# Kernel optimization log

Measured on AMD Instinct MI355X. Metric: run time of the kernel, lower is better.

The kernel has to match this reference:

```python
import jax, jax.numpy as jnp
import numpy as np

# --- config constants (from init_kwargs) ---
ALPHA = 0.05; SIGMA = 0.2; THETA = 0.3; A = 0.02; B_PAR = 0.1; RHO = 0.5
MULT = 2.0          # config.x_range_final[1]
GAMMA = 0.5         # power-utility exponent: u(x,r)=r*x^g/g, ux=r*x^(g-1)
N_STEPS = 100; T_FINAL = 1.0; DT = T_FINAL / N_STEPS
HID = 64; BATCH = 16384
PEN_SCALE = 100.0; LOWER = 1e-6


def _mlp(W1, b1, W2, b2, W3, b3, s):
    # tiny FeedForwardSubNet: 3 -> HID -> HID -> 1, tanh activations
    h = jnp.tanh(s @ W1 + b1)
    h = jnp.tanh(h @ W2 + b2)
    return h @ W3 + b3


def _penalise(v):
    # penalise_range(v, lower): quadratic hinge below `lower`
    return PEN_SCALE * jnp.square(jnp.maximum(LOWER - v, 0.0))


def setup_inputs() -> dict:
    key = jax.random.key(0)
    ks = jax.random.split(key, 16)
    dw = jax.random.normal(ks[0], (BATCH, 1, N_STEPS), dtype=jnp.float32) * float(np.sqrt(DT))
    X0 = jnp.ones((1,), jnp.float32)
    R0 = jnp.ones((1,), jnp.float32)
    def w(k, shape, fan):
        return jax.random.normal(k, shape, jnp.float32) / np.float32(np.sqrt(fan))
    inp = {"dw": dw, "X0": X0, "R0": R0,
           "pW1": w(ks[1], (3, HID), 3), "pb1": jnp.zeros((HID,), jnp.float32),
           "pW2": w(ks[2], (HID, HID), HID), "pb2": jnp.zeros((HID,), jnp.float32),
           "pW3": w(ks[3], (HID, 1), HID), "pb3": jnp.zeros((1,), jnp.float32),
           "qW1": w(ks[4], (3, HID), 3), "qb1": jnp.zeros((HID,), jnp.float32),
           "qW2": w(ks[5], (HID, HID), HID), "qb2": jnp.zeros((HID,), jnp.float32),
           "qW3": w(ks[6], (HID, 1), HID), "qb3": jnp.zeros((1,), jnp.float32)}
    return inp


def reference(dw, X0, R0, pW1, pb1, pW2, pb2, pW3, pb3, qW1, qb1, qW2, qb2, qW3, qb3):
    Bn = dw.shape[0]
    ones = jnp.ones((Bn, 1), dw.dtype)
    times = jnp.arange(N_STEPS + 1, dtype=dw.dtype) * DT   # [N+1]
    x0 = ones * X0
    R0v = ones * R0
    b_eff = float(np.sign(RHO)) * B_PAR

    # p_0 and dp_0 = d p_0 / d x (per-sample, rowwise independent net)
    def p_of_x(xx):
        st = jnp.concatenate([MULT * times[0] * ones, xx, R0v], 1)
        return _mlp(pW1, pb1, pW2, pb2, pW3, pb3, st)
    p0, p_vjp = jax.vjp(p_of_x, x0)
    (dp0,) = p_vjp(jnp.ones_like(p0))
    pi0 = _mlp(qW1, qb1, qW2, qb2, qW3, qb3,
               jnp.concatenate([MULT * times[0] * ones, x0, R0v], 1))

    dw_t = jnp.transpose(dw, (2, 0, 1))          # [N, B, 1]
    upd = jnp.arange(N_STEPS) < (N_STEPS - 1)    # pi not updated at last step

    def step(carry, inp):
        x, min_x, W, pi = carry
        dwi, t_next, u = inp
        x = x + x * ALPHA * DT + pi * SIGMA * THETA * DT + pi * SIGMA * dwi
        min_x = jnp.minimum(x, min_x)
        W = W + dwi
        Rv = R0v * jnp.exp((A - 0.5 * b_eff ** 2) * t_next + b_eff * W)
        p = p0 * jnp.exp(-(ALPHA + 0.5 * THETA ** 2) * t_next - THETA * W)
        st = jnp.concatenate([MULT * t_next * jnp.ones_like(x), x, Rv], 1)
        pi_new = _mlp(qW1, qb1, qW2, qb2, qW3, qb3, st)
        pi = jnp.where(u, pi_new, pi)
        return (x, min_x, W, pi), (x, Rv, pi, -p)

    (xf, min_x, Wf, pif), (xs, Rs, pis, dMs) = jax.lax.scan(
        step, (x0, x0, jnp.zeros_like(x0), pi0), (dw_t, times[1:], upd))

    # stacked process data, matching tf.concat-over-axis-0 ordering: [(N+1)*B, 1]
    x_all  = jnp.concatenate([x0[None], xs], 0).reshape(-1, 1)
    r_all  = jnp.concatenate([R0v[None], Rs], 0).reshape(-1, 1)
    pi_all = jnp.concatenate([pi0[None], pis], 0).reshape(-1, 1)
    dM_all = jnp.concatenate([(-p0)[None], dMs], 0).reshape(-1, 1)
    dM2_all = jnp.tile(-dp0, (N_STEPS + 1, 1))
    proc = jnp.concatenate([x_all, r_all, pi_all, dM_all, dM2_all], 1)  # [(N+1)*B, 5]

    # losses (non_concave = False branch)
    p_fin = -dMs[-1]
    R_fin = Rs[-1]
    xc = jnp.maximum(xf, LOWER)
    ux = R_fin * xc ** (GAMMA - 1.0)
    u_val = R_fin * xc ** GAMMA / GAMMA
    pen = _penalise(min_x)
    loss_p = jnp.mean(jnp.square(p_fin + ux) + pen)
    loss_pi = loss_p + jnp.mean(-u_val + pen)

    return jnp.concatenate([proc.reshape(-1), jnp.stack([loss_p, loss_pi])])
```

## Files before the change

### kernel.cpp

```cpp
#include <hip/hip_runtime.h>
#include <hip/hip_bf16.h>
#include <math.h>

#define NSTEP 100
#define BATCH 16384
#define MB 16
#define NBLK (BATCH/MB)
#define NT 64

#define C_ALPHA 0.05f
#define C_SIGMA 0.2f
#define C_THETA 0.3f
#define C_DT    0.01f
#define C_LOWER 1e-6f
#define C_PEN   100.0f
#define LOG2E   1.4426950408889634f
#define TSCALE  (2.0f * LOG2E)
#define CRT ( 0.015f * C_DT * LOG2E)
#define CRW ( 0.1f * LOG2E)
#define CPT (-0.095f * C_DT * LOG2E)
#define CPW (-0.3f * LOG2E)

typedef __attribute__((ext_vector_type(8))) short bf16x8;
typedef __attribute__((ext_vector_type(4))) float f32x4;

__device__ __forceinline__ float tanh_pre(float zs) {
    float e = __builtin_amdgcn_exp2f(zs);
    return 1.0f - 2.0f * __builtin_amdgcn_rcpf(e + 1.0f);
}
__device__ __forceinline__ unsigned f2bf_u(float f) {
    unsigned u = __float_as_uint(f);
    return (u + 0x7FFFu + ((u >> 16) & 1u)) >> 16;
}
__device__ __forceinline__ unsigned pack_bf16(float a, float b) {
    union { __hip_bfloat162 h; unsigned u; } cv;
    cv.h = __float22bfloat162_rn(make_float2(a, b));
    return cv.u;
}
__device__ __forceinline__ float dpp_row_sum16(float v) {
    int t;
    t = __builtin_amdgcn_update_dpp(0, __float_as_int(v), 0x128, 0xF, 0xF, true);
    v += __int_as_float(t);
    t = __builtin_amdgcn_update_dpp(0, __float_as_int(v), 0x124, 0xF, 0xF, true);
    v += __int_as_float(t);
    t = __builtin_amdgcn_update_dpp(0, __float_as_int(v), 0x122, 0xF, 0xF, true);
    v += __int_as_float(t);
    t = __builtin_amdgcn_update_dpp(0, __float_as_int(v), 0x121, 0xF, 0xF, true);
    v += __int_as_float(t);
    return v;
}

__global__ __launch_bounds__(NT, 1) void fused_kernel(
        const float* __restrict__ dw, const float* __restrict__ X0,
        const float* __restrict__ R0,
        const float* __restrict__ pW1, const float* __restrict__ pb1,
        const float* __restrict__ pW2, const float* __restrict__ pb2,
        const float* __restrict__ pW3, const float* __restrict__ pb3,
        const float* __restrict__ qW1, const float* __restrict__ qb1,
        const float* __restrict__ qW2, const float* __restrict__ qb2,
        const float* __restrict__ qW3, const float* __restrict__ qb3,
        float* __restrict__ ws, float* __restrict__ out) {
    __shared__ __align__(16) unsigned short sW2T[64 * 72];
    __shared__ __align__(16) float sdw[MB * NSTEP];

    const int tid = threadIdx.x;
    const int lane = tid;
    const int b0 = blockIdx.x * MB;
    const int l15 = lane & 15, quad = lane >> 4;

    {
        const float4* g = (const float4*)(dw + (size_t)b0 * NSTEP);
        float4* s = (float4*)sdw;
        for (int u = tid; u < MB * NSTEP / 4; u += NT) s[u] = g[u];
    }
    for (int u4 = tid; u4 < 1024; u4 += NT) {
        float4 w = ((const float4*)qW2)[u4];
        int base = u4 * 4;
        int k = base >> 6, n = base & 63;
        sW2T[(n + 0) * 72 + k] = (unsigned short)f2bf_u(w.x * TSCALE);
        sW2T[(n + 1) * 72 + k] = (unsigned short)f2bf_u(w.y * TSCALE);
        sW2T[(n + 2) * 72 + k] = (unsigned short)f2bf_u(w.z * TSCALE);
        sW2T[(n + 3) * 72 + k] = (unsigned short)f2bf_u(w.w * TSCALE);
    }
    __syncthreads();

    bf16x8 Bf[4][2];
    #pragma unroll
    for (int nt = 0; nt < 4; nt++) {
        const unsigned short* rp = &sW2T[(nt * 16 + l15) * 72 + quad * 8];
        Bf[nt][0] = *(const bf16x8*)rp;
        Bf[nt][1] = *(const bf16x8*)(rp + 32);
    }
    float tco[16], w1xs[16], w1rs[16], b1s[16];
    {
        const int kq = quad * 8;
        #pragma unroll
        for (int j = 0; j < 8; j++) {
            tco[j]      = qW1[kq + j]        * (2.0f * C_DT * TSCALE);
            tco[8 + j]  = qW1[32 + kq + j]   * (2.0f * C_DT * TSCALE);
            w1xs[j]     = qW1[64 + kq + j]   * TSCALE;
            w1xs[8 + j] = qW1[96 + kq + j]   * TSCALE;
            w1rs[j]     = qW1[128 + kq + j]  * TSCALE;
            w1rs[8 + j] = qW1[160 + kq + j]  * TSCALE;
            b1s[j]      = qb1[kq + j]        * TSCALE;
            b1s[8 + j]  = qb1[32 + kq + j]   * TSCALE;
        }
    }
    f32x4 b2a[4];
    float w3c[4][4];
    #pragma unroll
    for (int nt = 0; nt < 4; nt++) {
        #pragma unroll
        for (int r = 0; r < 4; r++) {
            b2a[nt][r] = qb2[nt * 16 + quad * 4 + r] * TSCALE;
            w3c[nt][r] = qW3[nt * 16 + quad * 4 + r];
        }
    }
    const float b3 = qb3[0];
    const float X0v = X0[0], R0s = R0[0];

    float p0, dp0;
    {
        float pre = fmaf(pW1[64 + lane], X0v, fmaf(pW1[128 + lane], R0s, pb1[lane]));
        float h1 = tanh_pre(TSCALE * pre);
        float d1 = (1.0f - h1 * h1) * pW1[64 + lane];
        float a0 = pb2[lane], a1 = 0.f, a2 = 0.f, a3 = 0.f;
        float e0 = 0.f, e1 = 0.f, e2 = 0.f, e3 = 0.f;
        for (int i2 = 0; i2 < 64; i2 += 4) {
            float w0 = pW2[(i2 + 0) * 64 + lane];
            float w1 = pW2[(i2 + 1) * 64 + lane];
            float w2 = pW2[(i2 + 2) * 64 + lane];
            float w3 = pW2[(i2 + 3) * 64 + lane];
            a0 = fmaf(__shfl(h1, i2 + 0), w0, a0); e0 = fmaf(__shfl(d1, i2 + 0), w0, e0);
            a1 = fmaf(__shfl(h1, i2 + 1), w1, a1); e1 = fmaf(__shfl(d1, i2 + 1), w1, e1);
            a2 = fmaf(__shfl(h1, i2 + 2), w2, a2); e2 = fmaf(__shfl(d1, i2 + 2), w2, e2);
            a3 = fmaf(__shfl(h1, i2 + 3), w3, a3); e3 = fmaf(__shfl(d1, i2 + 3), w3, e3);
        }
        float pre2 = (a0 + a1) + (a2 + a3);
        float dpre2 = (e0 + e1) + (e2 + e3);
        float h2 = tanh_pre(TSCALE * pre2);
        float d2 = (1.0f - h2 * h2) * dpre2;
        float c1 = h2 * pW3[lane], c2 = d2 * pW3[lane];
        #pragma unroll
        for (int o = 1; o < 64; o <<= 1) {
            c1 += __shfl_xor(c1, o);
            c2 += __shfl_xor(c2, o);
        }
        p0 = c1 + pb3[0]; dp0 = c2;
    }

    auto qnet = [&](float fi, float xv, float rv) -> float {
        union { bf16x8 v; unsigned u[4]; } A0u, A1u;
        #pragma unroll
        for (int p = 0; p < 4; p++) {
            const int i0 = 2 * p, i1 = 2 * p + 1;
            float z0 = fmaf(w1rs[i0], rv, fmaf(w1xs[i0], xv, fmaf(tco[i0], fi, b1s[i0])));
            float z1 = fmaf(w1rs[i1], rv, fmaf(w1xs[i1], xv, fmaf(tco[i1], fi, b1s[i1])));
            A0u.u[p] = pack_bf16(tanh_pre(z0), tanh_pre(z1));
            float z2 = fmaf(w1rs[8 + i0], rv, fmaf(w1xs[8 + i0], xv, fmaf(tco[8 + i0], fi, b1s[8 + i0])));
            float z3 = fmaf(w1rs[8 + i1], rv, fmaf(w1xs[8 + i1], xv, fmaf(tco[8 + i1], fi, b1s[8 + i1])));
            A1u.u[p] = pack_bf16(tanh_pre(z2), tanh_pre(z3));
        }
        float ps0 = 0.f, ps1 = 0.f, ps2 = 0.f, ps3 = 0.f;
        #pragma unroll
        for (int nt = 0; nt < 4; nt++) {
            f32x4 a = b2a[nt];
            a = __builtin_amdgcn_mfma_f32_16x16x32_bf16(Bf[nt][0], A0u.v, a, 0, 0, 0);
            a = __builtin_amdgcn_mfma_f32_16x16x32_bf16(Bf[nt][1], A1u.v, a, 0, 0, 0);
            ps0 = fmaf(tanh_pre(a[0]), w3c[nt][0], ps0);
            ps1 = fmaf(tanh_pre(a[1]), w3c[nt][1], ps1);
            ps2 = fmaf(tanh_pre(a[2]), w3c[nt][2], ps2);
            ps3 = fmaf(tanh_pre(a[3]), w3c[nt][3], ps3);
        }
        float ps = (ps0 + ps1) + (ps2 + ps3);
        ps += __shfl_xor(ps, 16);
        ps += __shfl_xor(ps, 32);
        return ps + b3;
    };

    float x = X0v, Wsum = 0.0f, minx = X0v;
    float pi = qnet(0.0f, X0v, R0s);
    if (quad == 0) {
        size_t base = (size_t)(b0 + l15) * 5;
        out[base] = X0v; out[base + 1] = R0s; out[base + 2] = pi;
        out[base + 3] = -p0; out[base + 4] = -dp0;
    }

    float dw_next = sdw[l15 * NSTEP];
    #pragma unroll 1
    for (int i = 0; i < NSTEP - 1; i++) {
        const float fi = (float)(i + 1);
        float dwv = dw_next;
        dw_next = sdw[l15 * NSTEP + i + 1];
        float t = pi * C_SIGMA;
        x = fmaf(x, 1.0f + C_ALPHA * C_DT, fmaf(t, dwv, t * (C_THETA * C_DT)));
        minx = fminf(minx, x);
        Wsum += dwv;
        float R = R0s * __builtin_amdgcn_exp2f(fmaf(CRW, Wsum, CRT * fi));
        float pm = p0 * __builtin_amdgcn_exp2f(fmaf(CPW, Wsum, CPT * fi));
        float pin = qnet(fi, x, R);
        if (quad == 0) {
            size_t base = ((size_t)(i + 1) * BATCH + b0 + l15) * 5;
            out[base] = x; out[base + 1] = R; out[base + 2] = pin;
            out[base + 3] = -pm; out[base + 4] = -dp0;
        }
        pi = pin;
    }

    {
        float dwv = dw_next;
        float t = pi * C_SIGMA;
        x = fmaf(x, 1.0f + C_ALPHA * C_DT, fmaf(t, dwv, t * (C_THETA * C_DT)));
        minx = fminf(minx, x);
        Wsum += dwv;
        float Rf = R0s * __builtin_amdgcn_exp2f(fmaf(CRW, Wsum, CRT * (float)NSTEP));
        float pf = p0 * __builtin_amdgcn_exp2f(fmaf(CPW, Wsum, CPT * (float)NSTEP));
        if (quad == 0) {
            size_t base = ((size_t)NSTEP * BATCH + b0 + l15) * 5;
            out[base] = x; out[base + 1] = Rf; out[base + 2] = pi;
            out[base + 3] = -pf; out[base + 4] = -dp0;
        }
        float xc = fmaxf(x, C_LOWER);
        float ux = Rf * rsqrtf(xc);
        float uval = 2.0f * Rf * sqrtf(xc);
        float d = fmaxf(C_LOWER - minx, 0.0f);
        float pen = C_PEN * d * d;
        float t1 = pf + ux;
        float v1 = dpp_row_sum16(t1 * t1 + pen);
        float v2 = dpp_row_sum16(-uval + pen);
        if (lane == 0) {
            atomicAdd(&ws[3], v1);
            atomicAdd(&ws[4], v2);
            __threadfence();
            int old = atomicAdd((int*)(ws + 5), 1);
            if (old == NBLK - 1) {
                float lp = atomicAdd(&ws[3], 0.0f) * (1.0f / (float)BATCH);
                float lq = atomicAdd(&ws[4], 0.0f) * (1.0f / (float)BATCH);
                out[(size_t)(NSTEP + 1) * BATCH * 5] = lp;
                out[(size_t)(NSTEP + 1) * BATCH * 5 + 1] = lp + lq;
            }
        }
    }
}

extern "C" void kernel_launch(void* const* d_in, const int* in_sizes, int n_in,
                              void* d_out, int out_size, void* d_ws, size_t ws_size,
                              hipStream_t stream) {
    const float* dw  = (const float*)d_in[0];
    const float* X0  = (const float*)d_in[1];
    const float* R0  = (const float*)d_in[2];
    const float* pW1 = (const float*)d_in[3];
    const float* pb1 = (const float*)d_in[4];
    const float* pW2 = (const float*)d_in[5];
    const float* pb2 = (const float*)d_in[6];
    const float* pW3 = (const float*)d_in[7];
    const float* pb3 = (const float*)d_in[8];
    const float* qW1 = (const float*)d_in[9];
    const float* qb1 = (const float*)d_in[10];
    const float* qW2 = (const float*)d_in[11];
    const float* qb2 = (const float*)d_in[12];
    const float* qW3 = (const float*)d_in[13];
    const float* qb3 = (const float*)d_in[14];
    float* out = (float*)d_out;
    float* ws  = (float*)d_ws;

    hipMemsetAsync(d_ws, 0, 64, stream);
    fused_kernel<<<NBLK, NT, 0, stream>>>(dw, X0, R0, pW1, pb1, pW2, pb2, pW3, pb3,
                                          qW1, qb1, qW2, qb2, qW3, qb3, ws, out);
}
```

Baseline: 215.1 us.

## Split per-step Q-network across two wavefronts with LDS exchange

```diff
diff --git a/kernel.cpp b/kernel.cpp
--- a/kernel.cpp
+++ b/kernel.cpp
@@ -6,7 +6,7 @@
 #define BATCH 16384
 #define MB 16
 #define NBLK (BATCH/MB)
-#define NT 64
+#define NT 128
 
 #define C_ALPHA 0.05f
 #define C_SIGMA 0.2f
@@ -21,6 +21,8 @@
 #define CPT (-0.095f * C_DT * LOG2E)
 #define CPW (-0.3f * LOG2E)
 
+#define WG_BARRIER() asm volatile("s_waitcnt lgkmcnt(0)\n\ts_barrier" ::: "memory")
+
 typedef __attribute__((ext_vector_type(8))) short bf16x8;
 typedef __attribute__((ext_vector_type(4))) float f32x4;
 
@@ -50,7 +52,7 @@
     return v;
 }
 
-__global__ __launch_bounds__(NT, 1) void fused_kernel(
+__global__ __launch_bounds__(NT, 2) void fused_kernel(
         const float* __restrict__ dw, const float* __restrict__ X0,
         const float* __restrict__ R0,
         const float* __restrict__ pW1, const float* __restrict__ pb1,
@@ -62,59 +64,48 @@
         float* __restrict__ ws, float* __restrict__ out) {
     __shared__ __align__(16) unsigned short sW2T[64 * 72];
     __shared__ __align__(16) float sdw[MB * NSTEP];
+    __shared__ __align__(16) uint4 sA[2][2][64];
+    __shared__ __align__(16) float sP[2][2][16];
 
     const int tid = threadIdx.x;
-    const int lane = tid;
+    const int lane = tid & 63;
+    const int wv = tid >> 6;
     const int b0 = blockIdx.x * MB;
     const int l15 = lane & 15, quad = lane >> 4;
 
     {
         const float4* g = (const float4*)(dw + (size_t)b0 * NSTEP);
         float4* s = (float4*)sdw;
+        #pragma unroll
         for (int u = tid; u < MB * NSTEP / 4; u += NT) s[u] = g[u];
     }
-    for (int u4 = tid; u4 < 1024; u4 += NT) {
-        float4 w = ((const float4*)qW2)[u4];
-        int base = u4 * 4;
-        int k = base >> 6, n = base & 63;
-        sW2T[(n + 0) * 72 + k] = (unsigned short)f2bf_u(w.x * TSCALE);
-        sW2T[(n + 1) * 72 + k] = (unsigned short)f2bf_u(w.y * TSCALE);
-        sW2T[(n + 2) * 72 + k] = (unsigned short)f2bf_u(w.z * TSCALE);
-        sW2T[(n + 3) * 72 + k] = (unsigned short)f2bf_u(w.w * TSCALE);
+    for (int u = tid; u < 4096; u += NT) {
+        int k = u >> 6, n = u & 63;
+        sW2T[n * 72 + k] = (unsigned short)f2bf_u(qW2[u] * TSCALE);
     }
     __syncthreads();
 
-    bf16x8 Bf[4][2];
+    bf16x8 Bf[2][2];
     #pragma unroll
-    for (int nt = 0; nt < 4; nt++) {
-        const unsigned short* rp = &sW2T[(nt * 16 + l15) * 72 + quad * 8];
-        Bf[nt][0] = *(const bf16x8*)rp;
-        Bf[nt][1] = *(const bf16x8*)(rp + 32);
-    }
-    float tco[16], w1xs[16], w1rs[16], b1s[16];
-    {
-        const int kq = quad * 8;
-        #pragma unroll
-        for (int j = 0; j < 8; j++) {
-            tco[j]      = qW1[kq + j]        * (2.0f * C_DT * TSCALE);
-            tco[8 + j]  = qW1[32 + kq + j]   * (2.0f * C_DT * TSCALE);
-            w1xs[j]     = qW1[64 + kq + j]   * TSCALE;
-            w1xs[8 + j] = qW1[96 + kq + j]   * TSCALE;
-            w1rs[j]     = qW1[128 + kq + j]  * TSCALE;
-            w1rs[8 + j] = qW1[160 + kq + j]  * TSCALE;
-            b1s[j]      = qb1[kq + j]        * TSCALE;
-            b1s[8 + j]  = qb1[32 + kq + j]   * TSCALE;
-        }
-    }
-    f32x4 b2a[4];
-    float w3c[4][4];
+    for (int t = 0; t < 2; t++) {
+        const unsigned short* r = &sW2T[(wv * 32 + t * 16 + l15) * 72 + quad * 8];
+        Bf[t][0] = *(const bf16x8*)r;
+        Bf[t][1] = *(const bf16x8*)(r + 32);
+    }
+    float tco[8], w1xs[8], w1rs[8], b1s[8];
     #pragma unroll
-    for (int nt = 0; nt < 4; nt++) {
-        #pragma unroll
-        for (int r = 0; r < 4; r++) {
-            b2a[nt][r] = qb2[nt * 16 + quad * 4 + r] * TSCALE;
-            w3c[nt][r] = qW3[nt * 16 + quad * 4 + r];
-        }
+    for (int j = 0; j < 8; j++) {
+        int k = wv * 32 + quad * 8 + j;
+        tco[j]  = qW1[k] * (2.0f * C_DT * TSCALE);
+        w1xs[j] = qW1[64 + k] * TSCALE;
+        w1rs[j] = qW1[128 + k] * TSCALE;
+        b1s[j]  = qb1[k] * TSCALE;
+    }
+    float b2v[2], w3v[2];
+    #pragma unroll
+    for (int t = 0; t < 2; t++) {
+        b2v[t] = qb2[wv * 32 + t * 16 + l15] * TSCALE;
+        w3v[t] = qW3[wv * 32 + t * 16 + l15];
     }
     const float b3 = qb3[0];
     const float X0v = X0[0], R0s = R0[0];
@@ -149,38 +140,39 @@
         p0 = c1 + pb3[0]; dp0 = c2;
     }
 
-    auto qnet = [&](float fi, float xv, float rv) -> float {
-        union { bf16x8 v; unsigned u[4]; } A0u, A1u;
+    auto qnet = [&](int par, float fi, float xv, float rv) -> float {
+        union { uint4 u4; bf16x8 v; unsigned u[4]; } Aloc, Aoth;
         #pragma unroll
         for (int p = 0; p < 4; p++) {
             const int i0 = 2 * p, i1 = 2 * p + 1;
             float z0 = fmaf(w1rs[i0], rv, fmaf(w1xs[i0], xv, fmaf(tco[i0], fi, b1s[i0])));
             float z1 = fmaf(w1rs[i1], rv, fmaf(w1xs[i1], xv, fmaf(tco[i1], fi, b1s[i1])));
-            A0u.u[p] = pack_bf16(tanh_pre(z0), tanh_pre(z1));
-            float z2 = fmaf(w1rs[8 + i0], rv, fmaf(w1xs[8 + i0], xv, fmaf(tco[8 + i0], fi, b1s[8 + i0])));
-            float z3 = fmaf(w1rs[8 + i1], rv, fmaf(w1xs[8 + i1], xv, fmaf(tco[8 + i1], fi, b1s[8 + i1])));
-            A1u.u[p] = pack_bf16(tanh_pre(z2), tanh_pre(z3));
-        }
-        float ps0 = 0.f, ps1 = 0.f, ps2 = 0.f, ps3 = 0.f;
-        #pragma unroll
-        for (int nt = 0; nt < 4; nt++) {
-            f32x4 a = b2a[nt];
-            a = __builtin_amdgcn_mfma_f32_16x16x32_bf16(Bf[nt][0], A0u.v, a, 0, 0, 0);
-            a = __builtin_amdgcn_mfma_f32_16x16x32_bf16(Bf[nt][1], A1u.v, a, 0, 0, 0);
-            ps0 = fmaf(tanh_pre(a[0]), w3c[nt][0], ps0);
-            ps1 = fmaf(tanh_pre(a[1]), w3c[nt][1], ps1);
-            ps2 = fmaf(tanh_pre(a[2]), w3c[nt][2], ps2);
-            ps3 = fmaf(tanh_pre(a[3]), w3c[nt][3], ps3);
-        }
-        float ps = (ps0 + ps1) + (ps2 + ps3);
-        ps += __shfl_xor(ps, 16);
-        ps += __shfl_xor(ps, 32);
-        return ps + b3;
+            Aloc.u[p] = pack_bf16(tanh_pre(z0), tanh_pre(z1));
+        }
+        sA[par][wv][lane] = Aloc.u4;
+        WG_BARRIER();
+        Aoth.u4 = sA[par][1 - wv][lane];
+        bf16x8 A0 = (wv == 0) ? Aloc.v : Aoth.v;
+        bf16x8 A1 = (wv == 0) ? Aoth.v : Aloc.v;
+        f32x4 acc0 = {b2v[0], b2v[0], b2v[0], b2v[0]};
+        f32x4 acc1 = {b2v[1], b2v[1], b2v[1], b2v[1]};
+        acc0 = __builtin_amdgcn_mfma_f32_16x16x32_bf16(A0, Bf[0][0], acc0, 0, 0, 0);
+        acc1 = __builtin_amdgcn_mfma_f32_16x16x32_bf16(A0, Bf[1][0], acc1, 0, 0, 0);
+        acc0 = __builtin_amdgcn_mfma_f32_16x16x32_bf16(A1, Bf[0][1], acc0, 0, 0, 0);
+        acc1 = __builtin_amdgcn_mfma_f32_16x16x32_bf16(A1, Bf[1][1], acc1, 0, 0, 0);
+        f32x4 part;
+        #pragma unroll
+        for (int r = 0; r < 4; r++)
+            part[r] = dpp_row_sum16(
+                fmaf(tanh_pre(acc1[r]), w3v[1], tanh_pre(acc0[r]) * w3v[0]));
+        if (l15 == 0) *(f32x4*)&sP[par][wv][quad * 4] = part;
+        WG_BARRIER();
+        return sP[par][0][l15] + sP[par][1][l15] + b3;
     };
 
     float x = X0v, Wsum = 0.0f, minx = X0v;
-    float pi = qnet(0.0f, X0v, R0s);
-    if (quad == 0) {
+    float pi = qnet(0, 0.0f, X0v, R0s);
+    if (wv == 1 && quad == 0) {
         size_t base = (size_t)(b0 + l15) * 5;
         out[base] = X0v; out[base + 1] = R0s; out[base + 2] = pi;
         out[base + 3] = -p0; out[base + 4] = -dp0;
@@ -198,8 +190,8 @@
         Wsum += dwv;
         float R = R0s * __builtin_amdgcn_exp2f(fmaf(CRW, Wsum, CRT * fi));
         float pm = p0 * __builtin_amdgcn_exp2f(fmaf(CPW, Wsum, CPT * fi));
-        float pin = qnet(fi, x, R);
-        if (quad == 0) {
+        float pin = qnet((i + 1) & 1, fi, x, R);
+        if (wv == 1 && quad == 0) {
             size_t base = ((size_t)(i + 1) * BATCH + b0 + l15) * 5;
             out[base] = x; out[base + 1] = R; out[base + 2] = pin;
             out[base + 3] = -pm; out[base + 4] = -dp0;
@@ -215,29 +207,31 @@
         Wsum += dwv;
         float Rf = R0s * __builtin_amdgcn_exp2f(fmaf(CRW, Wsum, CRT * (float)NSTEP));
         float pf = p0 * __builtin_amdgcn_exp2f(fmaf(CPW, Wsum, CPT * (float)NSTEP));
-        if (quad == 0) {
+        if (wv == 1 && quad == 0) {
             size_t base = ((size_t)NSTEP * BATCH + b0 + l15) * 5;
             out[base] = x; out[base + 1] = Rf; out[base + 2] = pi;
             out[base + 3] = -pf; out[base + 4] = -dp0;
         }
-        float xc = fmaxf(x, C_LOWER);
-        float ux = Rf * rsqrtf(xc);
-        float uval = 2.0f * Rf * sqrtf(xc);
-        float d = fmaxf(C_LOWER - minx, 0.0f);
-        float pen = C_PEN * d * d;
-        float t1 = pf + ux;
-        float v1 = dpp_row_sum16(t1 * t1 + pen);
-        float v2 = dpp_row_sum16(-uval + pen);
-        if (lane == 0) {
-            atomicAdd(&ws[3], v1);
-            atomicAdd(&ws[4], v2);
-            __threadfence();
-            int old = atomicAdd((int*)(ws + 5), 1);
-            if (old == NBLK - 1) {
-                float lp = atomicAdd(&ws[3], 0.0f) * (1.0f / (float)BATCH);
-                float lq = atomicAdd(&ws[4], 0.0f) * (1.0f / (float)BATCH);
-                out[(size_t)(NSTEP + 1) * BATCH * 5] = lp;
-                out[(size_t)(NSTEP + 1) * BATCH * 5 + 1] = lp + lq;
+        if (wv == 0) {
+            float xc = fmaxf(x, C_LOWER);
+            float ux = Rf * rsqrtf(xc);
+            float uval = 2.0f * Rf * sqrtf(xc);
+            float d = fmaxf(C_LOWER - minx, 0.0f);
+            float pen = C_PEN * d * d;
+            float t1 = pf + ux;
+            float v1 = dpp_row_sum16(t1 * t1 + pen);
+            float v2 = dpp_row_sum16(-uval + pen);
+            if (lane == 0) {
+                atomicAdd(&ws[3], v1);
+                atomicAdd(&ws[4], v2);
+                __threadfence();
+                int old = atomicAdd((int*)(ws + 5), 1);
+                if (old == NBLK - 1) {
+                    float lp = atomicAdd(&ws[3], 0.0f) * (1.0f / (float)BATCH);
+                    float lq = atomicAdd(&ws[4], 0.0f) * (1.0f / (float)BATCH);
+                    out[(size_t)(NSTEP + 1) * BATCH * 5] = lp;
+                    out[(size_t)(NSTEP + 1) * BATCH * 5 + 1] = lp + lq;
+                }
             }
         }
     }
```

After: 209.0 us. 1.03x faster.

## Replace tanh with LDS lookup table and make R/p updates incremental

Applied to the files above, without the earlier changes.

```diff
diff --git a/kernel.cpp b/kernel.cpp
--- a/kernel.cpp
+++ b/kernel.cpp
@@ -21,8 +21,15 @@
 #define CPT (-0.095f * C_DT * LOG2E)
 #define CPW (-0.3f * LOG2E)
 
+#define TSC   64.0f
+#define TOFF  512.0f
+#define TMAX  1023.999f
+#define AXD   (1.0f + C_ALPHA * C_DT)
+#define SIGTHDT (C_SIGMA * C_THETA * C_DT)
+
 typedef __attribute__((ext_vector_type(8))) short bf16x8;
 typedef __attribute__((ext_vector_type(4))) float f32x4;
+typedef __attribute__((ext_vector_type(4), aligned(4))) float f32x4a;
 
 __device__ __forceinline__ float tanh_pre(float zs) {
     float e = __builtin_amdgcn_exp2f(zs);
@@ -62,6 +69,7 @@
         float* __restrict__ ws, float* __restrict__ out) {
     __shared__ __align__(16) unsigned short sW2T[64 * 72];
     __shared__ __align__(16) float sdw[MB * NSTEP];
+    __shared__ __align__(16) float2 sTab[1024];
 
     const int tid = threadIdx.x;
     const int lane = tid;
@@ -77,12 +85,27 @@
         float4 w = ((const float4*)qW2)[u4];
         int base = u4 * 4;
         int k = base >> 6, n = base & 63;
-        sW2T[(n + 0) * 72 + k] = (unsigned short)f2bf_u(w.x * TSCALE);
-        sW2T[(n + 1) * 72 + k] = (unsigned short)f2bf_u(w.y * TSCALE);
-        sW2T[(n + 2) * 72 + k] = (unsigned short)f2bf_u(w.z * TSCALE);
-        sW2T[(n + 3) * 72 + k] = (unsigned short)f2bf_u(w.w * TSCALE);
+        sW2T[(n + 0) * 72 + k] = (unsigned short)f2bf_u(w.x * TSC);
+        sW2T[(n + 1) * 72 + k] = (unsigned short)f2bf_u(w.y * TSC);
+        sW2T[(n + 2) * 72 + k] = (unsigned short)f2bf_u(w.z * TSC);
+        sW2T[(n + 3) * 72 + k] = (unsigned short)f2bf_u(w.w * TSC);
+    }
+    for (int u = tid; u < 1024; u += NT) {
+        float z0 = (float)u * (1.0f / TSC) - 8.0f;
+        float t0 = tanh_pre(TSCALE * z0);
+        float t1 = tanh_pre(TSCALE * (z0 + 1.0f / TSC));
+        sTab[u] = make_float2(t0, t1 - t0);
     }
     __syncthreads();
+
+    auto tab = [&](float u) -> float {
+        u = fmaxf(u, 0.0f);
+        u = fminf(u, TMAX);
+        int idx = (int)u;
+        float f = u - (float)idx;
+        float2 e = sTab[idx];
+        return fmaf(f, e.y, e.x);
+    };
 
     bf16x8 Bf[4][2];
     #pragma unroll
@@ -96,14 +119,14 @@
         const int kq = quad * 8;
         #pragma unroll
         for (int j = 0; j < 8; j++) {
-            tco[j]      = qW1[kq + j]        * (2.0f * C_DT * TSCALE);
-            tco[8 + j]  = qW1[32 + kq + j]   * (2.0f * C_DT * TSCALE);
-            w1xs[j]     = qW1[64 + kq + j]   * TSCALE;
-            w1xs[8 + j] = qW1[96 + kq + j]   * TSCALE;
-            w1rs[j]     = qW1[128 + kq + j]  * TSCALE;
-            w1rs[8 + j] = qW1[160 + kq + j]  * TSCALE;
-            b1s[j]      = qb1[kq + j]        * TSCALE;
-            b1s[8 + j]  = qb1[32 + kq + j]   * TSCALE;
+            tco[j]      = qW1[kq + j]        * (2.0f * C_DT * TSC);
+            tco[8 + j]  = qW1[32 + kq + j]   * (2.0f * C_DT * TSC);
+            w1xs[j]     = qW1[64 + kq + j]   * TSC;
+            w1xs[8 + j] = qW1[96 + kq + j]   * TSC;
+            w1rs[j]     = qW1[128 + kq + j]  * TSC;
+            w1rs[8 + j] = qW1[160 + kq + j]  * TSC;
+            b1s[j]      = qb1[kq + j]        * TSC + TOFF;
+            b1s[8 + j]  = qb1[32 + kq + j]   * TSC + TOFF;
         }
     }
     f32x4 b2a[4];
@@ -112,7 +135,7 @@
     for (int nt = 0; nt < 4; nt++) {
         #pragma unroll
         for (int r = 0; r < 4; r++) {
-            b2a[nt][r] = qb2[nt * 16 + quad * 4 + r] * TSCALE;
+            b2a[nt][r] = qb2[nt * 16 + quad * 4 + r] * TSC + TOFF;
             w3c[nt][r] = qW3[nt * 16 + quad * 4 + r];
         }
     }
@@ -148,6 +171,7 @@
         }
         p0 = c1 + pb3[0]; dp0 = c2;
     }
+    const float mdp0 = -dp0;
 
     auto qnet = [&](float fi, float xv, float rv) -> float {
         union { bf16x8 v; unsigned u[4]; } A0u, A1u;
@@ -156,10 +180,10 @@
             const int i0 = 2 * p, i1 = 2 * p + 1;
             float z0 = fmaf(w1rs[i0], rv, fmaf(w1xs[i0], xv, fmaf(tco[i0], fi, b1s[i0])));
             float z1 = fmaf(w1rs[i1], rv, fmaf(w1xs[i1], xv, fmaf(tco[i1], fi, b1s[i1])));
-            A0u.u[p] = pack_bf16(tanh_pre(z0), tanh_pre(z1));
+            A0u.u[p] = pack_bf16(tab(z0), tab(z1));
             float z2 = fmaf(w1rs[8 + i0], rv, fmaf(w1xs[8 + i0], xv, fmaf(tco[8 + i0], fi, b1s[8 + i0])));
             float z3 = fmaf(w1rs[8 + i1], rv, fmaf(w1xs[8 + i1], xv, fmaf(tco[8 + i1], fi, b1s[8 + i1])));
-            A1u.u[p] = pack_bf16(tanh_pre(z2), tanh_pre(z3));
+            A1u.u[p] = pack_bf16(tab(z2), tab(z3));
         }
         float ps0 = 0.f, ps1 = 0.f, ps2 = 0.f, ps3 = 0.f;
         #pragma unroll
@@ -167,10 +191,10 @@
             f32x4 a = b2a[nt];
             a = __builtin_amdgcn_mfma_f32_16x16x32_bf16(Bf[nt][0], A0u.v, a, 0, 0, 0);
             a = __builtin_amdgcn_mfma_f32_16x16x32_bf16(Bf[nt][1], A1u.v, a, 0, 0, 0);
-            ps0 = fmaf(tanh_pre(a[0]), w3c[nt][0], ps0);
-            ps1 = fmaf(tanh_pre(a[1]), w3c[nt][1], ps1);
-            ps2 = fmaf(tanh_pre(a[2]), w3c[nt][2], ps2);
-            ps3 = fmaf(tanh_pre(a[3]), w3c[nt][3], ps3);
+            ps0 = fmaf(tab(a[0]), w3c[nt][0], ps0);
+            ps1 = fmaf(tab(a[1]), w3c[nt][1], ps1);
+            ps2 = fmaf(tab(a[2]), w3c[nt][2], ps2);
+            ps3 = fmaf(tab(a[3]), w3c[nt][3], ps3);
         }
         float ps = (ps0 + ps1) + (ps2 + ps3);
         ps += __shfl_xor(ps, 16);
@@ -178,12 +202,17 @@
         return ps + b3;
     };
 
-    float x = X0v, Wsum = 0.0f, minx = X0v;
+    float x = X0v, minx = X0v;
+    float R = R0s, pm = p0;
     float pi = qnet(0.0f, X0v, R0s);
-    if (quad == 0) {
+    {
         size_t base = (size_t)(b0 + l15) * 5;
-        out[base] = X0v; out[base + 1] = R0s; out[base + 2] = pi;
-        out[base + 3] = -p0; out[base + 4] = -dp0;
+        if (quad == 0) {
+            f32x4a o = {X0v, R0s, pi, -p0};
+            *(f32x4a*)(out + base) = o;
+        } else if (quad == 1) {
+            out[base + 4] = mdp0;
+        }
     }
 
     float dw_next = sdw[l15 * NSTEP];
@@ -192,33 +221,36 @@
         const float fi = (float)(i + 1);
         float dwv = dw_next;
         dw_next = sdw[l15 * NSTEP + i + 1];
-        float t = pi * C_SIGMA;
-        x = fmaf(x, 1.0f + C_ALPHA * C_DT, fmaf(t, dwv, t * (C_THETA * C_DT)));
+        R  *= __builtin_amdgcn_exp2f(fmaf(CRW, dwv, CRT));
+        pm *= __builtin_amdgcn_exp2f(fmaf(CPW, dwv, CPT));
+        float sp = fmaf(dwv, C_SIGMA, SIGTHDT);
+        x = fmaf(x, AXD, pi * sp);
         minx = fminf(minx, x);
-        Wsum += dwv;
-        float R = R0s * __builtin_amdgcn_exp2f(fmaf(CRW, Wsum, CRT * fi));
-        float pm = p0 * __builtin_amdgcn_exp2f(fmaf(CPW, Wsum, CPT * fi));
         float pin = qnet(fi, x, R);
+        size_t base = ((size_t)(i + 1) * BATCH + b0 + l15) * 5;
         if (quad == 0) {
-            size_t base = ((size_t)(i + 1) * BATCH + b0 + l15) * 5;
-            out[base] = x; out[base + 1] = R; out[base + 2] = pin;
-            out[base + 3] = -pm; out[base + 4] = -dp0;
+            f32x4a o = {x, R, pin, -pm};
+            *(f32x4a*)(out + base) = o;
+        } else if (quad == 1) {
+            out[base + 4] = mdp0;
         }
         pi = pin;
     }
 
     {
         float dwv = dw_next;
-        float t = pi * C_SIGMA;
-        x = fmaf(x, 1.0f + C_ALPHA * C_DT, fmaf(t, dwv, t * (C_THETA * C_DT)));
+        R  *= __builtin_amdgcn_exp2f(fmaf(CRW, dwv, CRT));
+        pm *= __builtin_amdgcn_exp2f(fmaf(CPW, dwv, CPT));
+        float sp = fmaf(dwv, C_SIGMA, SIGTHDT);
+        x = fmaf(x, AXD, pi * sp);
         minx = fminf(minx, x);
-        Wsum += dwv;
-        float Rf = R0s * __builtin_amdgcn_exp2f(fmaf(CRW, Wsum, CRT * (float)NSTEP));
-        float pf = p0 * __builtin_amdgcn_exp2f(fmaf(CPW, Wsum, CPT * (float)NSTEP));
+        float Rf = R, pf = pm;
+        size_t base = ((size_t)NSTEP * BATCH + b0 + l15) * 5;
         if (quad == 0) {
-            size_t base = ((size_t)NSTEP * BATCH + b0 + l15) * 5;
-            out[base] = x; out[base + 1] = Rf; out[base + 2] = pi;
-            out[base + 3] = -pf; out[base + 4] = -dp0;
+            f32x4a o = {x, Rf, pi, -pf};
+            *(f32x4a*)(out + base) = o;
+        } else if (quad == 1) {
+            out[base + 4] = mdp0;
         }
         float xc = fmaxf(x, C_LOWER);
         float ux = Rf * rsqrtf(xc);
```

After: 239.1 us. 1.11x slower.
